# Kernel tuning notes

Measured on AMD Instinct MI355X. Metric: run time of the kernel, lower is better.

The kernel has to match this reference:

```python
import jax, jax.numpy as jnp
import numpy as np

DIM = 512
NUM_HEADS = 8
HEAD_DIM = DIM // NUM_HEADS
EPS = 1e-05
BETA_INIT, TEMP_INIT, SHARP_INIT = 1.0, 0.5, 4.0


def setup_inputs() -> dict:
    key = jax.random.key(0)
    ks = jax.random.split(key, 9)
    b, t = 2, 1024
    s = 1.0 / np.sqrt(DIM)
    inp = {
        "x": jax.random.normal(ks[0], (b, t, DIM), dtype=jnp.float32),
        "wq_k": jax.random.normal(ks[1], (DIM, DIM), dtype=jnp.float32) * s,
        "wq_b": jnp.zeros((DIM,), dtype=jnp.float32),
        "wk_k": jax.random.normal(ks[2], (DIM, DIM), dtype=jnp.float32) * s,
        "wk_b": jnp.zeros((DIM,), dtype=jnp.float32),
        "wv_k": jax.random.normal(ks[3], (DIM, DIM), dtype=jnp.float32) * s,
        "wv_b": jnp.zeros((DIM,), dtype=jnp.float32),
        "wo_k": jax.random.normal(ks[4], (DIM, DIM), dtype=jnp.float32) * s,
        "wo_b": jnp.zeros((DIM,), dtype=jnp.float32),
        "log_beta": jnp.full((NUM_HEADS,), np.log(BETA_INIT), dtype=jnp.float32),
        "log_temp": jnp.full((NUM_HEADS,), np.log(TEMP_INIT), dtype=jnp.float32),
        "log_sharp": jnp.full((NUM_HEADS,), np.log(SHARP_INIT), dtype=jnp.float32),
    }
    return inp


def _softplus(x, beta):
    return (1.0 / beta) * jnp.log(1.0 + jnp.exp(beta * x))


def _combine(a, b):
    # log-domain combine: elements m (b,h,t,n), log_N (b,h,t,p,n), log_D (b,h,t,n)
    m_x, ln_x, ld_x = a
    m_y, ln_y, ld_y = b
    m_new = jnp.maximum(m_x, m_y)
    dx = m_x - m_new
    dy = m_y - m_new
    # note: (..., None) broadcast onto (b,h,t,p,n) works because p == n == HEAD_DIM
    ln_new = jnp.logaddexp(ln_x + dx[..., None], ln_y + dy[..., None])
    ld_new = jnp.logaddexp(ld_x + dx, ld_y + dy)
    return (m_new, ln_new, ld_new)


def reference(x, wq_k, wq_b, wk_k, wk_b, wv_k, wv_b, wo_k, wo_b,
              log_beta, log_temp, log_sharp):
    b, t, _ = x.shape
    q = (x @ wq_k + wq_b).reshape(b, t, NUM_HEADS, HEAD_DIM).transpose(0, 2, 1, 3)
    k = (x @ wk_k + wk_b).reshape(b, t, NUM_HEADS, HEAD_DIM).transpose(0, 2, 1, 3)
    v = (x @ wv_k + wv_b).reshape(b, t, NUM_HEADS, HEAD_DIM).transpose(0, 2, 1, 3)

    beta = jnp.exp(log_beta)[:, None, None]   # (h,1,1)
    temp = jnp.exp(log_temp)[:, None, None]
    sharp = jnp.exp(log_sharp)[:, None, None]

    q = q / temp
    k = k / temp
    Qf = _softplus(q, beta)  # (b,h,t,n)
    Kf = _softplus(k, beta)

    m0 = jnp.log(Kf + EPS)                         # (b,h,t,n)
    N0 = jnp.einsum('bhtp,bhtn->bhtpn', v, Kf)     # (b,h,t,p,n)
    D0 = Kf                                        # (b,h,t,n)

    m_c, N_c, D_c = jax.lax.associative_scan(_combine, (m0, N0, D0), axis=2)

    Y_num = jnp.einsum('bhtp,bhtpq->bhtq', Qf, N_c)
    Y_den = jnp.einsum('bhtp,bhtp->bht', Qf, D_c)
    Y = Y_num / (Y_den[..., None] + EPS)           # (b,h,t,n)
    Y = jnp.sign(Y) * jnp.abs(Y) ** sharp

    pos = (jnp.arange(1, t + 1, dtype=Y.dtype) / t).reshape(1, 1, t, 1)
    Y = Y * pos

    Y = Y.transpose(0, 2, 1, 3).reshape(b, t, DIM)
    return Y @ wo_k + wo_b
```

## Files before the change

kernel.cpp:

```cpp
#include <hip/hip_runtime.h>
#include <hip/hip_bf16.h>
#include <math.h>

#define DIM 512
#define NH 8
#define HD 64
#define TT 1024
#define CH 32
#define CL 32
#define EPSF 1e-5f
#define LN2F 0.69314718056f
#define LOG2EF 1.44269504089f

typedef unsigned short ushort_t;
typedef __attribute__((ext_vector_type(8))) short bf16x8;
typedef __attribute__((ext_vector_type(4))) float f32x4;

__device__ __forceinline__ float fexp2(float x) { return __builtin_amdgcn_exp2f(x); }
__device__ __forceinline__ float flog2(float x) { return __builtin_amdgcn_logf(x); }

__device__ __forceinline__ ushort_t f2bf(float f) {
    union { float f; unsigned u; } v; v.f = f;
    unsigned r = v.u + 0x7FFFu + ((v.u >> 16) & 1u);
    return (ushort_t)(r >> 16);
}
__device__ __forceinline__ float bf2f(ushort_t h) {
    union { unsigned u; float f; } v; v.u = ((unsigned)h) << 16;
    return v.f;
}

__launch_bounds__(256)
__global__ void k_cvt_x(const float* __restrict__ x, ushort_t* __restrict__ xh,
                        ushort_t* __restrict__ xl)
{
    int i = (blockIdx.x * 256 + threadIdx.x) * 4;
    float4 v = *(const float4*)&x[i];
    ushort4 h, l;
    h.x = f2bf(v.x); l.x = f2bf(v.x - bf2f(h.x));
    h.y = f2bf(v.y); l.y = f2bf(v.y - bf2f(h.y));
    h.z = f2bf(v.z); l.z = f2bf(v.z - bf2f(h.z));
    h.w = f2bf(v.w); l.w = f2bf(v.w - bf2f(h.w));
    *(ushort4*)&xh[i] = h;
    *(ushort4*)&xl[i] = l;
}

__launch_bounds__(256)
__global__ void k_cvt_w(const float* __restrict__ wq, const float* __restrict__ wk,
                        const float* __restrict__ wv, const float* __restrict__ wo,
                        ushort_t* __restrict__ wTh, ushort_t* __restrict__ wTl,
                        ushort_t* __restrict__ wTo)
{
    const int mat = blockIdx.z;
    const float* w = (mat == 0) ? wq : (mat == 1) ? wk : (mat == 2) ? wv : wo;
    const int n  = blockIdx.x * 64 + (threadIdx.x & 63);
    const int k0 = blockIdx.y * 128 + (threadIdx.x >> 6) * 32;

    ushort_t hb[32], lb[32];
#pragma unroll
    for (int j = 0; j < 32; j++) {
        float v = w[(size_t)(k0 + j) * DIM + n];
        hb[j] = f2bf(v);
        lb[j] = f2bf(v - bf2f(hb[j]));
    }
    if (mat < 3) {
        ushort_t* dh = wTh + (size_t)mat * DIM * DIM + (size_t)n * DIM + k0;
        ushort_t* dl = wTl + (size_t)mat * DIM * DIM + (size_t)n * DIM + k0;
#pragma unroll
        for (int j = 0; j < 8; j++) {
            ushort4 th = { hb[4*j], hb[4*j+1], hb[4*j+2], hb[4*j+3] };
            ushort4 tl = { lb[4*j], lb[4*j+1], lb[4*j+2], lb[4*j+3] };
            *(ushort4*)&dh[4*j] = th;
            *(ushort4*)&dl[4*j] = tl;
        }
    } else {
        ushort_t* dh = wTo + (size_t)n * DIM + k0;
#pragma unroll
        for (int j = 0; j < 8; j++) {
            ushort4 th = { hb[4*j], hb[4*j+1], hb[4*j+2], hb[4*j+3] };
            *(ushort4*)&dh[4*j] = th;
        }
    }
}

__launch_bounds__(256, 4)
__global__ void k_gemm_qkv(const ushort_t* __restrict__ xh, const ushort_t* __restrict__ xl,
                           const ushort_t* __restrict__ wTh, const ushort_t* __restrict__ wTl,
                           const float* __restrict__ bq, const float* __restrict__ bk,
                           const float* __restrict__ bv,
                           const float* __restrict__ lbeta, const float* __restrict__ ltemp,
                           float* __restrict__ Qf2, float* __restrict__ Kf,
                           float* __restrict__ Vv2)
{
    const int z = blockIdx.z, h = blockIdx.x;
    const int rowBase = blockIdx.y * 64;
    const int colBase = h * 64;
    const float* bias = (z == 0) ? bq : (z == 1) ? bk : bv;

    __shared__ __align__(16) ushort_t lds[2][4][2048];

    const int tid = threadIdx.x;
    const int l = tid & 63, wv = tid >> 6;
    const int m = l & 15, g = l >> 4;

    const int rl = tid >> 2, cc = tid & 3;
    const int ci = ((rl >> 4) * 64 + cc * 16 + (rl & 15)) * 8;
    const ushort_t* gAh = xh + (size_t)(rowBase + rl) * DIM + cc * 8;
    const ushort_t* gAl = xl + (size_t)(rowBase + rl) * DIM + cc * 8;
    const ushort_t* gBh = wTh + (size_t)z * DIM * DIM + (size_t)(colBase + rl) * DIM + cc * 8;
    const ushort_t* gBl = wTl + (size_t)z * DIM * DIM + (size_t)(colBase + rl) * DIM + cc * 8;

    f32x4 acc[4] = { {0,0,0,0}, {0,0,0,0}, {0,0,0,0}, {0,0,0,0} };

    {
        bf16x8 a0 = *(const bf16x8*)gAh;
        bf16x8 a1 = *(const bf16x8*)gAl;
        bf16x8 b0 = *(const bf16x8*)gBh;
        bf16x8 b1 = *(const bf16x8*)gBl;
        *(bf16x8*)&lds[0][0][ci] = a0;
        *(bf16x8*)&lds[0][1][ci] = a1;
        *(bf16x8*)&lds[0][2][ci] = b0;
        *(bf16x8*)&lds[0][3][ci] = b1;
    }
    __syncthreads();

    for (int it = 0; it < 16; ++it) {
        const int cur = it & 1;
        bf16x8 nAh, nAl, nBh, nBl;
        if (it < 15) {
            const int K = (it + 1) * 32;
            nAh = *(const bf16x8*)(gAh + K);
            nAl = *(const bf16x8*)(gAl + K);
            nBh = *(const bf16x8*)(gBh + K);
            nBl = *(const bf16x8*)(gBl + K);
        }
        bf16x8 ah = *(const bf16x8*)&lds[cur][0][tid * 8];
        bf16x8 al = *(const bf16x8*)&lds[cur][1][tid * 8];
#pragma unroll
        for (int n = 0; n < 4; n++) {
            bf16x8 bh = *(const bf16x8*)&lds[cur][2][(n * 64 + l) * 8];
            bf16x8 bl = *(const bf16x8*)&lds[cur][3][(n * 64 + l) * 8];
            acc[n] = __builtin_amdgcn_mfma_f32_16x16x32_bf16(ah, bh, acc[n], 0, 0, 0);
            acc[n] = __builtin_amdgcn_mfma_f32_16x16x32_bf16(al, bh, acc[n], 0, 0, 0);
            acc[n] = __builtin_amdgcn_mfma_f32_16x16x32_bf16(ah, bl, acc[n], 0, 0, 0);
        }
        if (it < 15) {
            const int nxt = cur ^ 1;
            *(bf16x8*)&lds[nxt][0][ci] = nAh;
            *(bf16x8*)&lds[nxt][1][ci] = nAl;
            *(bf16x8*)&lds[nxt][2][ci] = nBh;
            *(bf16x8*)&lds[nxt][3][ci] = nBl;
            __syncthreads();
        }
    }

    if (z == 2) {
#pragma unroll
        for (int n = 0; n < 4; n++) {
            int c = n * 16 + m;
            float bval = bias[colBase + c];
#pragma unroll
            for (int r = 0; r < 4; r++) {
                int rr = rowBase + wv * 16 + g * 4 + r;
                int bb = rr >> 10, t = rr & (TT - 1);
                Vv2[(((size_t)(bb * NH + h)) * TT + t) * HD + c] = (acc[n][r] + bval) * LOG2EF;
            }
        }
    } else {
        float beta = expf(lbeta[h]);
        float itemp = 1.0f / expf(ltemp[h]);
        float oscale = (z == 0) ? (LN2F / beta) : (1.0f / beta);
        float* __restrict__ dst = (z == 0) ? Qf2 : Kf;
#pragma unroll
        for (int n = 0; n < 4; n++) {
            int c = n * 16 + m;
            float bval = bias[colBase + c];
#pragma unroll
            for (int r = 0; r < 4; r++) {
                int rr = rowBase + wv * 16 + g * 4 + r;
                int bb = rr >> 10, t = rr & (TT - 1);
                float val = (acc[n][r] + bval) * itemp;
                float zz = beta * val;
                float sp = (fmaxf(zz, 0.f) + log1pf(expf(-fabsf(zz)))) * oscale;
                dst[(((size_t)(bb * NH + h)) * TT + t) * HD + c] = sp;
            }
        }
    }
}

__launch_bounds__(256)
__global__ void k_chunk_reduce(const float* __restrict__ Kf, const float* __restrict__ Vv2,
                               float* __restrict__ aA, float* __restrict__ aD,
                               float* __restrict__ aCM)
{
    const int c = blockIdx.x >> 1, qh = blockIdx.x & 1;
    const int bh = blockIdx.z * NH + blockIdx.y;
    const int tid = threadIdx.x;

    __shared__ __align__(16) float sK[CL * HD];
    __shared__ __align__(16) float sV2[CL * HD];
    __shared__ __align__(16) float sM02[CL * HD];

    size_t base = ((size_t)bh * TT + (size_t)c * CL) * HD;
    const float4* K4 = (const float4*)(Kf + base);
    const float4* V4 = (const float4*)(Vv2 + base);
#pragma unroll
    for (int r = 0; r < 2; r++) {
        int f = tid + 256 * r;
        float4 kv = K4[f];
        ((float4*)sK)[f] = kv;
        float4 mm;
        mm.x = flog2(kv.x + EPSF); mm.y = flog2(kv.y + EPSF);
        mm.z = flog2(kv.z + EPSF); mm.w = flog2(kv.w + EPSF);
        ((float4*)sM02)[f] = mm;
        ((float4*)sV2)[f] = V4[f];
    }
    __syncthreads();

    const int p = tid & 63, qo = tid >> 6;
    const int q0 = qh * 32 + qo * 8;
    float A[8] = {};
    float AD = 0.f, cmx = 0.f;
    const bool doD = (qh == 0) && (tid < 64);

    for (int s = 0; s < CL; s++) {
        float vp = sV2[s * HD + p];
        float mp = sM02[s * HD + p];
        float4 ka = *(const float4*)&sK[s * HD + q0];
        float4 kb = *(const float4*)&sK[s * HD + q0 + 4];
        A[0] += fexp2(fmaf(vp, ka.x, mp));
        A[1] += fexp2(fmaf(vp, ka.y, mp));
        A[2] += fexp2(fmaf(vp, ka.z, mp));
        A[3] += fexp2(fmaf(vp, ka.w, mp));
        A[4] += fexp2(fmaf(vp, kb.x, mp));
        A[5] += fexp2(fmaf(vp, kb.y, mp));
        A[6] += fexp2(fmaf(vp, kb.z, mp));
        A[7] += fexp2(fmaf(vp, kb.w, mp));
        if (doD) {
            float kn = sK[s * HD + tid];
            float mn = sM02[s * HD + tid];
            AD += fexp2(fmaf(kn, LOG2EF, mn));
            cmx = fmaxf(cmx, kn + EPSF);
        }
    }

    size_t abase = ((size_t)bh * CH + c) * 4096 + (size_t)p * HD + q0;
    float4 o0 = { A[0], A[1], A[2], A[3] };
    float4 o1 = { A[4], A[5], A[6], A[7] };
    *(float4*)&aA[abase] = o0;
    *(float4*)&aA[abase + 4] = o1;
    if (doD) {
        size_t dbase = ((size_t)bh * CH + c) * HD + tid;
        aD[dbase] = AD; aCM[dbase] = cmx;
    }
}

__global__ void k_scan_agg(float* __restrict__ aA, float* __restrict__ aD,
                           float* __restrict__ aCM, int BH)
{
    int idx = blockIdx.x * 256 + threadIdx.x;
    int nA = BH * 4096, nD = BH * 64;
    if (idx < nA) {
        int bh = idx >> 12, pn = idx & 4095;
        float Sr = 0.f;
        for (int c = 0; c < CH; c++) {
            size_t off = ((size_t)bh * CH + c) * 4096 + pn;
            float t = aA[off]; aA[off] = Sr; Sr += t;
        }
    } else if (idx < nA + nD) {
        int i = idx - nA; int bh = i >> 6, n = i & 63;
        float Sr = 0.f;
        for (int c = 0; c < CH; c++) {
            size_t off = ((size_t)bh * CH + c) * HD + n;
            float t = aD[off]; aD[off] = Sr; Sr += t;
        }
    } else if (idx < nA + 2 * nD) {
        int i = idx - nA - nD; int bh = i >> 6, n = i & 63;
        float r = 0.f;
        for (int c = 0; c < CH; c++) {
            size_t off = ((size_t)bh * CH + c) * HD + n;
            float v = aCM[off]; aCM[off] = r; r = fmaxf(r, v);
        }
    }
}

__launch_bounds__(64)
__global__ void k_den(const float* __restrict__ Kf, const float* __restrict__ Qf2,
                      const float* __restrict__ aD, const float* __restrict__ aCM,
                      float* __restrict__ c1f, float* __restrict__ invd)
{
    const int c = blockIdx.x;
    const int bh = blockIdx.z * NH + blockIdx.y;
    const int n = threadIdx.x;
    size_t dbase = ((size_t)bh * CH + c) * HD + n;
    float AD = aD[dbase], cmx = aCM[dbase];
    size_t base = ((size_t)bh * TT + (size_t)c * CL) * HD + n;
    float* outc = c1f + (size_t)bh * TT + c * CL;
    float* outi = invd + (size_t)bh * TT + c * CL;

    for (int s = 0; s < CL; s++) {
        float kn = Kf[base + (size_t)s * HD];
        float qn = Qf2[base + (size_t)s * HD];
        float mn = flog2(kn + EPSF);
        AD += fexp2(fmaf(kn, LOG2EF, mn));
        cmx = fmaxf(cmx, kn + EPSF);
        float t1 = qn * flog2(cmx);
        float t2 = qn * flog2(AD);
#pragma unroll
        for (int off = 1; off <= 32; off <<= 1) {
            t1 += __shfl_xor(t1, off);
            t2 += __shfl_xor(t2, off);
        }
        if (n == 0) {
            outc[s] = t1;
            outi[s] = 1.0f / (t2 - t1 + EPSF);
        }
    }
}

__launch_bounds__(256)
__global__ void k_chunk_out(const float* __restrict__ Kf, const float* __restrict__ Vv2,
                            const float* __restrict__ Qf2, const float* __restrict__ aA,
                            const float* __restrict__ c1f, const float* __restrict__ invd,
                            const float* __restrict__ lsharp, ushort_t* __restrict__ Ymb)
{
    const int c = blockIdx.x, hh = blockIdx.y, bb = blockIdx.z;
    const int bh = bb * NH + hh;
    const int tid = threadIdx.x;

    __shared__ __align__(16) float sK[CL * HD];
    __shared__ __align__(16) float sV2[CL * HD];
    __shared__ __align__(16) float sM02[CL * HD];
    __shared__ __align__(16) float sQ2[CL * HD];

    size_t base = ((size_t)bh * TT + (size_t)c * CL) * HD;
    const float4* K4 = (const float4*)(Kf + base);
    const float4* V4 = (const float4*)(Vv2 + base);
    const float4* Q4 = (const float4*)(Qf2 + base);
#pragma unroll
    for (int r = 0; r < 2; r++) {
        int f = tid + 256 * r;
        float4 kv = K4[f];
        ((float4*)sK)[f] = kv;
        float4 mm;
        mm.x = flog2(kv.x + EPSF); mm.y = flog2(kv.y + EPSF);
        mm.z = flog2(kv.z + EPSF); mm.w = flog2(kv.w + EPSF);
        ((float4*)sM02)[f] = mm;
        ((float4*)sV2)[f] = V4[f];
        ((float4*)sQ2)[f] = Q4[f];
    }
    __syncthreads();

    const int lane = tid & 63, w = tid >> 6;
    const int g = lane >> 3, qil = lane & 7;
    const int qA = w * 8 + qil, qB = qA + 32;
    const int p0 = g * 8;

    float A[8], Bq[8];
    size_t abase = ((size_t)bh * CH + c) * 4096;
#pragma unroll
    for (int j = 0; j < 8; j++) {
        A[j]  = aA[abase + (size_t)(p0 + j) * HD + qA];
        Bq[j] = aA[abase + (size_t)(p0 + j) * HD + qB];
    }
    const float sharp = expf(lsharp[hh]);
    const float invT = 1.0f / (float)TT;
    const float* c1p = c1f + (size_t)bh * TT + c * CL;
    const float* ivp = invd + (size_t)bh * TT + c * CL;

    for (int s = 0; s < CL; s++) {
        float kqA = sK[s * HD + qA];
        float kqB = sK[s * HD + qB];
        float partA = 0.f, partB = 0.f;
#pragma unroll
        for (int j4 = 0; j4 < 2; j4++) {
            float4 vv = *(const float4*)&sV2[s * HD + p0 + j4 * 4];
            float4 mm = *(const float4*)&sM02[s * HD + p0 + j4 * 4];
            float4 qv = *(const float4*)&sQ2[s * HD + p0 + j4 * 4];
#define STEP(comp, jj) { \
            A[jj]  += fexp2(fmaf(vv.comp, kqA, mm.comp)); \
            partA = fmaf(qv.comp, flog2(A[jj]), partA); \
            Bq[jj] += fexp2(fmaf(vv.comp, kqB, mm.comp)); \
            partB = fmaf(qv.comp, flog2(Bq[jj]), partB); }
            STEP(x, j4 * 4 + 0)
            STEP(y, j4 * 4 + 1)
            STEP(z, j4 * 4 + 2)
            STEP(w, j4 * 4 + 3)
#undef STEP
        }
        partA += __shfl_xor(partA, 8);
        partA += __shfl_xor(partA, 16);
        partA += __shfl_xor(partA, 32);
        partB += __shfl_xor(partB, 8);
        partB += __shfl_xor(partB, 16);
        partB += __shfl_xor(partB, 32);

        float c1v = c1p[s], iv = ivp[s];
        int tg = c * CL + s;
        float scale = (float)(tg + 1) * invT;
        float yA = (partA - c1v) * iv;
        float yB = (partB - c1v) * iv;
        float oA = copysignf(fexp2(sharp * flog2(fabsf(yA))), yA) * scale;
        float oB = copysignf(fexp2(sharp * flog2(fabsf(yB))), yB) * scale;
        if (g == 0) {
            ushort_t* yrow = Ymb + ((size_t)(bb * TT + tg)) * DIM + hh * HD;
            yrow[qA] = f2bf(oA);
            yrow[qB] = f2bf(oB);
        }
    }
}

__launch_bounds__(256, 4)
__global__ void k_gemm_out(const ushort_t* __restrict__ Ymb, const ushort_t* __restrict__ wTo,
                           const float* __restrict__ bias, float* __restrict__ out)
{
    const int colBase = blockIdx.x * 64;
    const int rowBase = blockIdx.y * 32;

    __shared__ __align__(16) ushort_t sA[2][1024];
    __shared__ __align__(16) ushort_t sB[2][2048];

    const int tid = threadIdx.x;
    const int l = tid & 63, wv = tid >> 6;
    const int m = l & 15, g = l >> 4;
    const int wr = wv & 1, wc = wv >> 1;

    const int rlB = tid >> 2, ccB = tid & 3;
    const int ciB = ((rlB >> 4) * 64 + ccB * 16 + (rlB & 15)) * 8;
    const ushort_t* gB = wTo + (size_t)(colBase + rlB) * DIM + ccB * 8;
    const int rlA = (tid & 127) >> 2, ccA = tid & 3;
    const int ciA = ((rlA >> 4) * 64 + ccA * 16 + (rlA & 15)) * 8;
    const ushort_t* gA = Ymb + (size_t)(rowBase + rlA) * DIM + ccA * 8;
    const bool doA = tid < 128;

    f32x4 acc[2] = { {0,0,0,0}, {0,0,0,0} };

    {
        bf16x8 b0 = *(const bf16x8*)gB;
        *(bf16x8*)&sB[0][ciB] = b0;
        if (doA) {
            bf16x8 a0 = *(const bf16x8*)gA;
            *(bf16x8*)&sA[0][ciA] = a0;
        }
    }
    __syncthreads();

    for (int it = 0; it < 16; ++it) {
        const int cur = it & 1;
        bf16x8 nA, nB;
        if (it < 15) {
            const int K = (it + 1) * 32;
            nB = *(const bf16x8*)(gB + K);
            if (doA) nA = *(const bf16x8*)(gA + K);
        }
        bf16x8 a = *(const bf16x8*)&sA[cur][(wr * 64 + l) * 8];
#pragma unroll
        for (int n = 0; n < 2; n++) {
            bf16x8 b = *(const bf16x8*)&sB[cur][((wc * 2 + n) * 64 + l) * 8];
            acc[n] = __builtin_amdgcn_mfma_f32_16x16x32_bf16(a, b, acc[n], 0, 0, 0);
        }
        if (it < 15) {
            const int nxt = cur ^ 1;
            *(bf16x8*)&sB[nxt][ciB] = nB;
            if (doA) *(bf16x8*)&sA[nxt][ciA] = nA;
            __syncthreads();
        }
    }

#pragma unroll
    for (int n = 0; n < 2; n++) {
        int c = colBase + wc * 32 + n * 16 + m;
        float bval = bias[c];
#pragma unroll
        for (int r = 0; r < 4; r++) {
            int rr = rowBase + wr * 16 + g * 4 + r;
            out[(size_t)rr * DIM + c] = acc[n][r] + bval;
        }
    }
}

extern "C" void kernel_launch(void* const* d_in, const int* in_sizes, int n_in,
                              void* d_out, int out_size, void* d_ws, size_t ws_size,
                              hipStream_t stream)
{
    const float* x  = (const float*)d_in[0];
    const float* wq = (const float*)d_in[1];
    const float* bq = (const float*)d_in[2];
    const float* wk = (const float*)d_in[3];
    const float* bk = (const float*)d_in[4];
    const float* wv = (const float*)d_in[5];
    const float* bv = (const float*)d_in[6];
    const float* wo = (const float*)d_in[7];
    const float* bo = (const float*)d_in[8];
    const float* lb = (const float*)d_in[9];
    const float* lt = (const float*)d_in[10];
    const float* ls = (const float*)d_in[11];

    const int B  = in_sizes[0] / (TT * DIM);
    const int BH = B * NH;

    float* ws = (float*)d_ws;
    const size_t nQ = (size_t)BH * TT * HD;
    float* Qf2 = ws;
    float* Kf  = Qf2 + nQ;
    float* Vv2 = Kf + nQ;
    float* region = Vv2 + nQ;

    ushort_t* xh  = (ushort_t*)region;
    ushort_t* xl  = xh + (size_t)B * TT * DIM;
    ushort_t* wTh = (ushort_t*)(region + (size_t)B * TT * DIM);
    ushort_t* wTl = wTh + (size_t)3 * DIM * DIM;
    ushort_t* Ymb = (ushort_t*)region;
    float* aA  = region + (size_t)B * TT * DIM;
    float* aD  = aA  + (size_t)BH * CH * 4096;
    float* aCM = aD  + (size_t)BH * CH * HD;
    float* c1f = aCM + (size_t)BH * CH * HD;
    float* invd= c1f + (size_t)BH * TT;
    ushort_t* wTo = (ushort_t*)(invd + (size_t)BH * TT);

    k_cvt_x<<<(B * TT * DIM) / 1024, 256, 0, stream>>>(x, xh, xl);

    dim3 gw(DIM / 64, DIM / 128, 4);
    k_cvt_w<<<gw, 256, 0, stream>>>(wq, wk, wv, wo, wTh, wTl, wTo);

    dim3 g1(NH, (B * TT) / 64, 3);
    k_gemm_qkv<<<g1, 256, 0, stream>>>(xh, xl, wTh, wTl, bq, bk, bv, lb, lt, Qf2, Kf, Vv2);

    dim3 g2(CH * 2, NH, B);
    k_chunk_reduce<<<g2, 256, 0, stream>>>(Kf, Vv2, aA, aD, aCM);

    int ntot = BH * 4096 + 2 * BH * 64;
    k_scan_agg<<<(ntot + 255) / 256, 256, 0, stream>>>(aA, aD, aCM, BH);

    dim3 g4(CH, NH, B);
    k_den<<<g4, 64, 0, stream>>>(Kf, Qf2, aD, aCM, c1f, invd);

    k_chunk_out<<<g4, 256, 0, stream>>>(Kf, Vv2, Qf2, aA, c1f, invd, ls, Ymb);

    dim3 g6(DIM / 64, (B * TT) / 32);
    k_gemm_out<<<g6, 256, 0, stream>>>(Ymb, wTo, bo, (float*)d_out);
}
```

Measured before the change: 105.8 us.

## Halve scan chunk length, vectorize chunk-prefix scan, split FMA accumulators

Changes the chunked scan from 32 chunks of 32 steps to 64 chunks of 16 steps. This doubles the number of blocks in the chunk-reduce and chunk-output kernels and halves the serial per-chunk loop, at the cost of a longer serial prefix over chunks and a larger aggregate buffer. The cross-chunk prefix kernel now processes float4 per thread, using a quarter as many threads with 128-bit memory accesses. The output kernel splits each partial dot-product accumulator into two to shorten the FMA dependency chains.

```diff
diff --git a/kernel.cpp b/kernel.cpp
--- a/kernel.cpp
+++ b/kernel.cpp
@@ -6,8 +6,8 @@
 #define NH 8
 #define HD 64
 #define TT 1024
-#define CH 32
-#define CL 32
+#define CH 64
+#define CL 16
 #define EPSF 1e-5f
 #define LN2F 0.69314718056f
 #define LOG2EF 1.44269504089f
@@ -203,9 +203,8 @@
     size_t base = ((size_t)bh * TT + (size_t)c * CL) * HD;
     const float4* K4 = (const float4*)(Kf + base);
     const float4* V4 = (const float4*)(Vv2 + base);
-#pragma unroll
-    for (int r = 0; r < 2; r++) {
-        int f = tid + 256 * r;
+    {
+        int f = tid;
         float4 kv = K4[f];
         ((float4*)sK)[f] = kv;
         float4 mm;
@@ -258,27 +257,35 @@
                            float* __restrict__ aCM, int BH)
 {
     int idx = blockIdx.x * 256 + threadIdx.x;
-    int nA = BH * 4096, nD = BH * 64;
-    if (idx < nA) {
-        int bh = idx >> 12, pn = idx & 4095;
-        float Sr = 0.f;
+    int nA4 = BH * 1024;
+    int nD4 = BH * 16;
+    if (idx < nA4) {
+        int bh = idx >> 10, pn4 = (idx & 1023) * 4;
+        float4 Sr = {0.f, 0.f, 0.f, 0.f};
         for (int c = 0; c < CH; c++) {
-            size_t off = ((size_t)bh * CH + c) * 4096 + pn;
-            float t = aA[off]; aA[off] = Sr; Sr += t;
-        }
-    } else if (idx < nA + nD) {
-        int i = idx - nA; int bh = i >> 6, n = i & 63;
-        float Sr = 0.f;
+            float* p = &aA[((size_t)bh * CH + c) * 4096 + pn4];
+            float4 t = *(float4*)p;
+            *(float4*)p = Sr;
+            Sr.x += t.x; Sr.y += t.y; Sr.z += t.z; Sr.w += t.w;
+        }
+    } else if (idx < nA4 + nD4) {
+        int i = idx - nA4; int bh = i >> 4, n4 = (i & 15) * 4;
+        float4 Sr = {0.f, 0.f, 0.f, 0.f};
         for (int c = 0; c < CH; c++) {
-            size_t off = ((size_t)bh * CH + c) * HD + n;
-            float t = aD[off]; aD[off] = Sr; Sr += t;
-        }
-    } else if (idx < nA + 2 * nD) {
-        int i = idx - nA - nD; int bh = i >> 6, n = i & 63;
-        float r = 0.f;
+            float* p = &aD[((size_t)bh * CH + c) * HD + n4];
+            float4 t = *(float4*)p;
+            *(float4*)p = Sr;
+            Sr.x += t.x; Sr.y += t.y; Sr.z += t.z; Sr.w += t.w;
+        }
+    } else if (idx < nA4 + 2 * nD4) {
+        int i = idx - nA4 - nD4; int bh = i >> 4, n4 = (i & 15) * 4;
+        float4 r = {0.f, 0.f, 0.f, 0.f};
         for (int c = 0; c < CH; c++) {
-            size_t off = ((size_t)bh * CH + c) * HD + n;
-            float v = aCM[off]; aCM[off] = r; r = fmaxf(r, v);
+            float* p = &aCM[((size_t)bh * CH + c) * HD + n4];
+            float4 t = *(float4*)p;
+            *(float4*)p = r;
+            r.x = fmaxf(r.x, t.x); r.y = fmaxf(r.y, t.y);
+            r.z = fmaxf(r.z, t.z); r.w = fmaxf(r.w, t.w);
         }
     }
 }
@@ -336,9 +343,8 @@
     const float4* K4 = (const float4*)(Kf + base);
     const float4* V4 = (const float4*)(Vv2 + base);
     const float4* Q4 = (const float4*)(Qf2 + base);
-#pragma unroll
-    for (int r = 0; r < 2; r++) {
-        int f = tid + 256 * r;
+    {
+        int f = tid;
         float4 kv = K4[f];
         ((float4*)sK)[f] = kv;
         float4 mm;
@@ -370,23 +376,25 @@
     for (int s = 0; s < CL; s++) {
         float kqA = sK[s * HD + qA];
         float kqB = sK[s * HD + qB];
-        float partA = 0.f, partB = 0.f;
+        float pA0 = 0.f, pA1 = 0.f, pB0 = 0.f, pB1 = 0.f;
 #pragma unroll
         for (int j4 = 0; j4 < 2; j4++) {
             float4 vv = *(const float4*)&sV2[s * HD + p0 + j4 * 4];
             float4 mm = *(const float4*)&sM02[s * HD + p0 + j4 * 4];
             float4 qv = *(const float4*)&sQ2[s * HD + p0 + j4 * 4];
-#define STEP(comp, jj) { \
+#define STEP(comp, jj, PA, PB) { \
             A[jj]  += fexp2(fmaf(vv.comp, kqA, mm.comp)); \
-            partA = fmaf(qv.comp, flog2(A[jj]), partA); \
+            PA = fmaf(qv.comp, flog2(A[jj]), PA); \
             Bq[jj] += fexp2(fmaf(vv.comp, kqB, mm.comp)); \
-            partB = fmaf(qv.comp, flog2(Bq[jj]), partB); }
-            STEP(x, j4 * 4 + 0)
-            STEP(y, j4 * 4 + 1)
-            STEP(z, j4 * 4 + 2)
-            STEP(w, j4 * 4 + 3)
+            PB = fmaf(qv.comp, flog2(Bq[jj]), PB); }
+            STEP(x, j4 * 4 + 0, pA0, pB0)
+            STEP(y, j4 * 4 + 1, pA1, pB1)
+            STEP(z, j4 * 4 + 2, pA0, pB0)
+            STEP(w, j4 * 4 + 3, pA1, pB1)
 #undef STEP
         }
+        float partA = pA0 + pA1;
+        float partB = pB0 + pB1;
         partA += __shfl_xor(partA, 8);
         partA += __shfl_xor(partA, 16);
         partA += __shfl_xor(partA, 32);
@@ -528,7 +536,7 @@
     dim3 g2(CH * 2, NH, B);
     k_chunk_reduce<<<g2, 256, 0, stream>>>(Kf, Vv2, aA, aD, aCM);
 
-    int ntot = BH * 4096 + 2 * BH * 64;
+    int ntot = BH * 1024 + 2 * BH * 16;
     k_scan_agg<<<(ntot + 255) / 256, 256, 0, stream>>>(aA, aD, aCM, BH);
 
     dim3 g4(CH, NH, B);
```

Result: faster. 98.63 us (-6.8%).
